# Kernel optimization log

Measured on AMD Instinct MI355X. Metric: run time of the kernel, lower is better.

The kernel has to match this reference:

```python
import jax, jax.numpy as jnp
import numpy as np

B, H, P, L = 16, 128, 64, 8192  # batch, d_input, d_state, seq_len
TWO_PI = 6.283185307179586


def setup_inputs() -> dict:
    key = jax.random.key(0)
    k_u, k_lr, k_li, k_br, k_bi, k_cr, k_ci, k_d = jax.random.split(key, 8)
    u = jax.random.normal(k_u, (B, H, L), dtype=jnp.float32)
    # continuous-time diagonal state matrix: Lambda = -rand + i*2*pi*rand
    lam_re = -jax.random.uniform(k_lr, (P,), dtype=jnp.float32)
    lam_im = TWO_PI * jax.random.uniform(k_li, (P,), dtype=jnp.float32)
    Lam = lam_re + 1j * lam_im                       # (P,) complex64
    Lambda_bar = jnp.exp(Lam)                        # ZOH with Delta=1
    # continuous B, then ZOH: B_bar = (Lambda_bar - 1)/Lambda * B
    Bc = (jax.random.normal(k_br, (P, H), dtype=jnp.float32)
          + 1j * jax.random.normal(k_bi, (P, H), dtype=jnp.float32))
    B_bar = ((Lambda_bar - 1.0) / Lam)[:, None] * Bc  # (P,H) complex64
    C = (jax.random.normal(k_cr, (H, P), dtype=jnp.float32)
         + 1j * jax.random.normal(k_ci, (H, P), dtype=jnp.float32))
    D = jax.random.normal(k_d, (H, H), dtype=jnp.float32)
    return {
        "u": u,
        "Lambda_re": jnp.real(Lambda_bar).astype(jnp.float32),
        "Lambda_im": jnp.imag(Lambda_bar).astype(jnp.float32),
        "B_re": jnp.real(B_bar).astype(jnp.float32),
        "B_im": jnp.imag(B_bar).astype(jnp.float32),
        "C_re": jnp.real(C).astype(jnp.float32),
        "C_im": jnp.imag(C).astype(jnp.float32),
        "D": D,
    }


def _binary_op(elem_i, elem_j):
    # diagonal linear recurrence combine: (A^i, Bu_i) o (A^j, Bu_j)
    a_i, bu_i = elem_i
    a_j, bu_j = elem_j
    return a_j * a_i, a_j * bu_i + bu_j


def reference(u, Lambda_re, Lambda_im, B_re, B_im, C_re, C_im, D):
    Lambda_bar = Lambda_re + 1j * Lambda_im           # (P,)
    B_bar = B_re + 1j * B_im                          # (P,H)
    C = C_re + 1j * C_im                              # (H,P)
    uc = u.astype(B_bar.dtype)                        # (B,H,L) complex
    Bu = jnp.einsum('ph,bhl->bpl', B_bar, uc)         # (B,P,L)
    A = jnp.broadcast_to(Lambda_bar[None, :, None], Bu.shape)
    # parallel associative scan of the diagonal linear recurrence over L
    _, xs = jax.lax.associative_scan(_binary_op, (A, Bu), axis=2)  # (B,P,L)
    C_A_Bu = jnp.einsum('hp,bpl->bhl', C, xs).real    # (B,H,L)
    # einsum('hh,bhl->bhl', D, u) uses only the diagonal of D
    Du = jnp.diagonal(D)[None, :, None] * u           # (B,H,L)
    return jax.nn.gelu(C_A_Bu + Du, approximate=False)
```

## Files before the change

kernel.cpp:

```cpp
#include <hip/hip_runtime.h>
#include <math.h>

#define NB 16
#define NH 128
#define NP 64
#define NL 8192

__global__ __launch_bounds__(256) void k_bu(
    const float* __restrict__ u, const float* __restrict__ Bre,
    const float* __restrict__ Bim, float2* __restrict__ bu) {
  __shared__ float sBre[32][68];
  __shared__ float sBim[32][68];
  __shared__ float sU[32][128];
  const int b  = blockIdx.y;
  const int l0 = blockIdx.x * 128;
  const int t  = threadIdx.x;
  const int tp = t & 15;
  const int tl = t >> 4;
  float accRe[4][8], accIm[4][8];
  #pragma unroll
  for (int i = 0; i < 4; ++i)
    #pragma unroll
    for (int j = 0; j < 8; ++j) { accRe[i][j] = 0.f; accIm[i][j] = 0.f; }

  for (int ht = 0; ht < 4; ++ht) {
    const int h0 = ht * 32;
    #pragma unroll
    for (int idx = t; idx < 2048; idx += 256) {
      int h = idx & 31, p = idx >> 5;
      sBre[h][p] = Bre[p * NH + h0 + h];
      sBim[h][p] = Bim[p * NH + h0 + h];
    }
    #pragma unroll
    for (int idx = t; idx < 32 * 128; idx += 256) {
      int l = idx & 127, h = idx >> 7;
      sU[h][l] = u[((size_t)(b * NH + h0 + h)) * NL + l0 + l];
    }
    __syncthreads();
    #pragma unroll 4
    for (int h = 0; h < 32; ++h) {
      float4 br4 = *(const float4*)&sBre[h][tp * 4];
      float4 bi4 = *(const float4*)&sBim[h][tp * 4];
      float4 ua  = *(const float4*)&sU[h][tl * 8];
      float4 ub  = *(const float4*)&sU[h][tl * 8 + 4];
      float uu[8] = {ua.x, ua.y, ua.z, ua.w, ub.x, ub.y, ub.z, ub.w};
      float brr[4] = {br4.x, br4.y, br4.z, br4.w};
      float bii[4] = {bi4.x, bi4.y, bi4.z, bi4.w};
      #pragma unroll
      for (int i = 0; i < 4; ++i)
        #pragma unroll
        for (int j = 0; j < 8; ++j) {
          accRe[i][j] = fmaf(brr[i], uu[j], accRe[i][j]);
          accIm[i][j] = fmaf(bii[i], uu[j], accIm[i][j]);
        }
    }
    __syncthreads();
  }
  #pragma unroll
  for (int i = 0; i < 4; ++i) {
    size_t base = ((size_t)(b * NP + tp * 4 + i)) * NL + l0 + tl * 8;
    #pragma unroll
    for (int j = 0; j < 8; j += 2) {
      float4 v = make_float4(accRe[i][j], accIm[i][j], accRe[i][j + 1], accIm[i][j + 1]);
      *(float4*)&bu[base + j] = v;
    }
  }
}

__global__ __launch_bounds__(256) void k_scan(
    float2* __restrict__ bu, const float* __restrict__ Lre,
    const float* __restrict__ Lim) {
  extern __shared__ float2 s[];
  const int bp = blockIdx.x;
  const int p  = bp & (NP - 1);
  const int t  = threadIdx.x;
  const size_t base = (size_t)bp * NL;

  float2 v[32];
  #pragma unroll
  for (int j = 0; j < 32; ++j) v[j] = bu[base + t + 256 * j];
  #pragma unroll
  for (int j = 0; j < 32; ++j) { int i = t + 256 * j; s[i + (i >> 5)] = v[j]; }
  __syncthreads();
  #pragma unroll
  for (int j = 0; j < 32; ++j) v[j] = s[t * 33 + j];

  const float lr = Lre[p], li = Lim[p];
  float xr = 0.f, xi = 0.f;
  #pragma unroll
  for (int j = 0; j < 32; ++j) {
    float nr = fmaf(lr, xr, fmaf(-li, xi, v[j].x));
    float ni = fmaf(lr, xi, fmaf( li, xr, v[j].y));
    xr = nr; xi = ni;
    v[j].x = xr; v[j].y = xi;
  }
  __syncthreads();

  float wr = lr, wi = li;
  #pragma unroll
  for (int k = 0; k < 5; ++k) { float nr = wr * wr - wi * wi; wi = 2.f * wr * wi; wr = nr; }
  float2 tot = v[31];
  s[t] = tot;
  __syncthreads();
  for (int d = 1; d < 256; d <<= 1) {
    float2 nb;
    if (t >= d) nb = s[t - d];
    __syncthreads();
    if (t >= d) {
      tot.x += wr * nb.x - wi * nb.y;
      tot.y += wr * nb.y + wi * nb.x;
      s[t] = tot;
    }
    __syncthreads();
    float nr = wr * wr - wi * wi; wi = 2.f * wr * wi; wr = nr;
  }
  float2 ep = (t > 0) ? s[t - 1] : make_float2(0.f, 0.f);
  __syncthreads();

  float cr = ep.x, ci = ep.y;
  #pragma unroll
  for (int j = 0; j < 32; ++j) {
    float nr = lr * cr - li * ci;
    float nc = lr * ci + li * cr;
    cr = nr; ci = nc;
    v[j].x += cr; v[j].y += ci;
  }
  #pragma unroll
  for (int j = 0; j < 32; ++j) s[t * 33 + j] = v[j];
  __syncthreads();
  #pragma unroll
  for (int j = 0; j < 32; ++j) { int i = t + 256 * j; bu[base + i] = s[i + (i >> 5)]; }
}

__global__ __launch_bounds__(256) void k_out(
    const float2* __restrict__ xs, const float* __restrict__ u,
    const float* __restrict__ Cre, const float* __restrict__ Cim,
    const float* __restrict__ D, float* __restrict__ out) {
  __shared__ float sCre[16][132];
  __shared__ float sCim[16][132];
  __shared__ float sXre[16][128];
  __shared__ float sXim[16][128];
  __shared__ float sDd[128];
  const int b  = blockIdx.y;
  const int l0 = blockIdx.x * 128;
  const int t  = threadIdx.x;
  const int lane = t & 63, w = t >> 6;
  const int th = (lane & 7) + 8 * (w & 1);
  const int tl = (lane >> 3) + 8 * (w >> 1);

  if (t < 128) sDd[t] = D[t * NH + t];

  float acc[8][8];
  #pragma unroll
  for (int i = 0; i < 8; ++i)
    #pragma unroll
    for (int j = 0; j < 8; ++j) acc[i][j] = 0.f;

  for (int pt = 0; pt < 4; ++pt) {
    const int p0 = pt * 16;
    __syncthreads();
    #pragma unroll
    for (int idx = t; idx < 2048; idx += 256) {
      int pp = idx & 15, h = idx >> 4;
      sCre[pp][h] = Cre[h * NP + p0 + pp];
      sCim[pp][h] = Cim[h * NP + p0 + pp];
    }
    #pragma unroll
    for (int idx = t; idx < 2048; idx += 256) {
      int l = idx & 127, pp = idx >> 7;
      float2 xv = xs[((size_t)(b * NP + p0 + pp)) * NL + l0 + l];
      sXre[pp][l] = xv.x; sXim[pp][l] = xv.y;
    }
    __syncthreads();
    #pragma unroll 4
    for (int pp = 0; pp < 16; ++pp) {
      float4 ca = *(const float4*)&sCre[pp][th * 8];
      float4 cb = *(const float4*)&sCre[pp][th * 8 + 4];
      float4 ia = *(const float4*)&sCim[pp][th * 8];
      float4 ib = *(const float4*)&sCim[pp][th * 8 + 4];
      float4 xa = *(const float4*)&sXre[pp][tl * 8];
      float4 xb = *(const float4*)&sXre[pp][tl * 8 + 4];
      float4 ya = *(const float4*)&sXim[pp][tl * 8];
      float4 yb = *(const float4*)&sXim[pp][tl * 8 + 4];
      float cr[8] = {ca.x, ca.y, ca.z, ca.w, cb.x, cb.y, cb.z, cb.w};
      float ci[8] = {ia.x, ia.y, ia.z, ia.w, ib.x, ib.y, ib.z, ib.w};
      float xr[8] = {xa.x, xa.y, xa.z, xa.w, xb.x, xb.y, xb.z, xb.w};
      float xi[8] = {ya.x, ya.y, ya.z, ya.w, yb.x, yb.y, yb.z, yb.w};
      #pragma unroll
      for (int i = 0; i < 8; ++i)
        #pragma unroll
        for (int j = 0; j < 8; ++j) {
          acc[i][j] = fmaf(cr[i], xr[j], acc[i][j]);
          acc[i][j] = fmaf(-ci[i], xi[j], acc[i][j]);
        }
    }
  }

  #pragma unroll
  for (int i = 0; i < 8; ++i) {
    const int h = th * 8 + i;
    const float dd = sDd[h];
    size_t rb = ((size_t)(b * NH + h)) * NL + l0 + tl * 8;
    float4 u0 = *(const float4*)&u[rb];
    float4 u1 = *(const float4*)&u[rb + 4];
    float uu[8] = {u0.x, u0.y, u0.z, u0.w, u1.x, u1.y, u1.z, u1.w};
    float r[8];
    #pragma unroll
    for (int j = 0; j < 8; ++j) {
      float vv = acc[i][j] + dd * uu[j];
      r[j] = 0.5f * vv * (1.0f + erff(vv * 0.70710678118654752f));
    }
    *(float4*)&out[rb]     = make_float4(r[0], r[1], r[2], r[3]);
    *(float4*)&out[rb + 4] = make_float4(r[4], r[5], r[6], r[7]);
  }
}

extern "C" void kernel_launch(void* const* d_in, const int* in_sizes, int n_in,
                              void* d_out, int out_size, void* d_ws, size_t ws_size,
                              hipStream_t stream) {
  (void)in_sizes; (void)n_in; (void)out_size; (void)ws_size;
  const float* u   = (const float*)d_in[0];
  const float* Lre = (const float*)d_in[1];
  const float* Lim = (const float*)d_in[2];
  const float* Bre = (const float*)d_in[3];
  const float* Bim = (const float*)d_in[4];
  const float* Cre = (const float*)d_in[5];
  const float* Cim = (const float*)d_in[6];
  const float* Dm  = (const float*)d_in[7];
  float* out = (float*)d_out;
  float2* bu = (float2*)d_ws;

  dim3 g1(NL / 128, NB);
  k_bu<<<g1, 256, 0, stream>>>(u, Bre, Bim, bu);
  k_scan<<<NB * NP, 256, 8448 * sizeof(float2), stream>>>(bu, Lre, Lim);
  dim3 g3(NL / 128, NB);
  k_out<<<g3, 256, 0, stream>>>(bu, u, Cre, Cim, Dm, out);
}
```

Measured before the change: 302.5 us.

## Fuse chunked local scan into Bu GEMM and apply carries in output kernel

Result: faster. 264.0 us (-12.7%).

```diff
diff --git a/kernel.cpp b/kernel.cpp
--- a/kernel.cpp
+++ b/kernel.cpp
@@ -5,15 +5,19 @@
 #define NH 128
 #define NP 64
 #define NL 8192
-
-__global__ __launch_bounds__(256) void k_bu(
+#define NCHUNK 64
+
+__global__ __launch_bounds__(256) void k_bu_scan(
     const float* __restrict__ u, const float* __restrict__ Bre,
-    const float* __restrict__ Bim, float2* __restrict__ bu) {
-  __shared__ float sBre[32][68];
+    const float* __restrict__ Bim, const float* __restrict__ Lre,
+    const float* __restrict__ Lim, float2* __restrict__ xloc,
+    float2* __restrict__ Echunk) {
+  __shared__ __align__(16) float sBre[32][68];
   __shared__ float sBim[32][68];
   __shared__ float sU[32][128];
   const int b  = blockIdx.y;
-  const int l0 = blockIdx.x * 128;
+  const int c  = blockIdx.x;
+  const int l0 = c * 128;
   const int t  = threadIdx.x;
   const int tp = t & 15;
   const int tl = t >> 4;
@@ -56,97 +60,138 @@
     }
     __syncthreads();
   }
+
+  float lr[4], li[4];
+  #pragma unroll
+  for (int i = 0; i < 4; ++i) { lr[i] = Lre[tp * 4 + i]; li[i] = Lim[tp * 4 + i]; }
+  #pragma unroll
+  for (int i = 0; i < 4; ++i) {
+    float xr = 0.f, xi = 0.f;
+    #pragma unroll
+    for (int j = 0; j < 8; ++j) {
+      float nr = fmaf(lr[i], xr, fmaf(-li[i], xi, accRe[i][j]));
+      float ni = fmaf(lr[i], xi, fmaf( li[i], xr, accIm[i][j]));
+      xr = nr; xi = ni; accRe[i][j] = xr; accIm[i][j] = xi;
+    }
+  }
+
+  float2* E = reinterpret_cast<float2*>(&sBre[0][0]);
+  #define EL(p, q) E[(p) * 17 + (q)]
+  #pragma unroll
+  for (int i = 0; i < 4; ++i)
+    EL(tp * 4 + i, tl) = make_float2(accRe[i][7], accIm[i][7]);
+
+  float wr[4], wi[4];
+  #pragma unroll
+  for (int i = 0; i < 4; ++i) {
+    float ar = lr[i], ai = li[i];
+    #pragma unroll
+    for (int k = 0; k < 3; ++k) { float nr = ar * ar - ai * ai; ai = 2.f * ar * ai; ar = nr; }
+    wr[i] = ar; wi[i] = ai;
+  }
+  __syncthreads();
+  #pragma unroll
+  for (int d = 1; d < 16; d <<= 1) {
+    float2 rv[4];
+    #pragma unroll
+    for (int i = 0; i < 4; ++i)
+      rv[i] = (tl >= d) ? EL(tp * 4 + i, tl - d) : make_float2(0.f, 0.f);
+    __syncthreads();
+    if (tl >= d) {
+      #pragma unroll
+      for (int i = 0; i < 4; ++i) {
+        float2 cur = EL(tp * 4 + i, tl);
+        cur.x += wr[i] * rv[i].x - wi[i] * rv[i].y;
+        cur.y += wr[i] * rv[i].y + wi[i] * rv[i].x;
+        EL(tp * 4 + i, tl) = cur;
+      }
+    }
+    __syncthreads();
+    #pragma unroll
+    for (int i = 0; i < 4; ++i) {
+      float nr = wr[i] * wr[i] - wi[i] * wi[i];
+      wi[i] = 2.f * wr[i] * wi[i]; wr[i] = nr;
+    }
+  }
+
+  float2 cin[4];
+  #pragma unroll
+  for (int i = 0; i < 4; ++i)
+    cin[i] = (tl > 0) ? EL(tp * 4 + i, tl - 1) : make_float2(0.f, 0.f);
+  if (t < 64) {
+    float2 tot = EL(t, 15);
+    Echunk[((size_t)(b * NCHUNK + c)) * NP + t] = tot;
+  }
+
+  #pragma unroll
+  for (int i = 0; i < 4; ++i) {
+    float cr = cin[i].x, ci = cin[i].y;
+    #pragma unroll
+    for (int j = 0; j < 8; ++j) {
+      float nr = lr[i] * cr - li[i] * ci;
+      float nc = lr[i] * ci + li[i] * cr;
+      cr = nr; ci = nc;
+      accRe[i][j] += cr; accIm[i][j] += ci;
+    }
+  }
+
   #pragma unroll
   for (int i = 0; i < 4; ++i) {
     size_t base = ((size_t)(b * NP + tp * 4 + i)) * NL + l0 + tl * 8;
     #pragma unroll
     for (int j = 0; j < 8; j += 2) {
       float4 v = make_float4(accRe[i][j], accIm[i][j], accRe[i][j + 1], accIm[i][j + 1]);
-      *(float4*)&bu[base + j] = v;
-    }
-  }
+      *(float4*)&xloc[base + j] = v;
+    }
+  }
+  #undef EL
 }
 
-__global__ __launch_bounds__(256) void k_scan(
-    float2* __restrict__ bu, const float* __restrict__ Lre,
-    const float* __restrict__ Lim) {
-  extern __shared__ float2 s[];
-  const int bp = blockIdx.x;
-  const int p  = bp & (NP - 1);
-  const int t  = threadIdx.x;
-  const size_t base = (size_t)bp * NL;
-
-  float2 v[32];
-  #pragma unroll
-  for (int j = 0; j < 32; ++j) v[j] = bu[base + t + 256 * j];
-  #pragma unroll
-  for (int j = 0; j < 32; ++j) { int i = t + 256 * j; s[i + (i >> 5)] = v[j]; }
-  __syncthreads();
-  #pragma unroll
-  for (int j = 0; j < 32; ++j) v[j] = s[t * 33 + j];
-
+__global__ void k_carry(const float2* __restrict__ Echunk,
+                        const float* __restrict__ Lre, const float* __restrict__ Lim,
+                        float2* __restrict__ carryg, float2* __restrict__ powtab) {
+  const int b = blockIdx.x, p = threadIdx.x;
   const float lr = Lre[p], li = Lim[p];
+  float wr = lr, wi = li;
+  #pragma unroll
+  for (int k = 0; k < 7; ++k) { float nr = wr * wr - wi * wi; wi = 2.f * wr * wi; wr = nr; }
   float xr = 0.f, xi = 0.f;
-  #pragma unroll
-  for (int j = 0; j < 32; ++j) {
-    float nr = fmaf(lr, xr, fmaf(-li, xi, v[j].x));
-    float ni = fmaf(lr, xi, fmaf( li, xr, v[j].y));
+  for (int c = 0; c < NCHUNK; ++c) {
+    carryg[((size_t)(b * NCHUNK + c)) * NP + p] = make_float2(xr, xi);
+    float2 e = Echunk[((size_t)(b * NCHUNK + c)) * NP + p];
+    float nr = e.x + wr * xr - wi * xi;
+    float ni = e.y + wr * xi + wi * xr;
     xr = nr; xi = ni;
-    v[j].x = xr; v[j].y = xi;
-  }
-  __syncthreads();
-
-  float wr = lr, wi = li;
-  #pragma unroll
-  for (int k = 0; k < 5; ++k) { float nr = wr * wr - wi * wi; wi = 2.f * wr * wi; wr = nr; }
-  float2 tot = v[31];
-  s[t] = tot;
-  __syncthreads();
-  for (int d = 1; d < 256; d <<= 1) {
-    float2 nb;
-    if (t >= d) nb = s[t - d];
-    __syncthreads();
-    if (t >= d) {
-      tot.x += wr * nb.x - wi * nb.y;
-      tot.y += wr * nb.y + wi * nb.x;
-      s[t] = tot;
-    }
-    __syncthreads();
-    float nr = wr * wr - wi * wi; wi = 2.f * wr * wi; wr = nr;
-  }
-  float2 ep = (t > 0) ? s[t - 1] : make_float2(0.f, 0.f);
-  __syncthreads();
-
-  float cr = ep.x, ci = ep.y;
-  #pragma unroll
-  for (int j = 0; j < 32; ++j) {
-    float nr = lr * cr - li * ci;
-    float nc = lr * ci + li * cr;
-    cr = nr; ci = nc;
-    v[j].x += cr; v[j].y += ci;
-  }
-  #pragma unroll
-  for (int j = 0; j < 32; ++j) s[t * 33 + j] = v[j];
-  __syncthreads();
-  #pragma unroll
-  for (int j = 0; j < 32; ++j) { int i = t + 256 * j; bu[base + i] = s[i + (i >> 5)]; }
+  }
+  if (b == 0) {
+    float pr = 1.f, pi = 0.f;
+    for (int j = 0; j < 128; ++j) {
+      float nr = pr * lr - pi * li;
+      pi = pr * li + pi * lr; pr = nr;
+      powtab[p * 128 + j] = make_float2(pr, pi);
+    }
+  }
 }
 
 __global__ __launch_bounds__(256) void k_out(
     const float2* __restrict__ xs, const float* __restrict__ u,
     const float* __restrict__ Cre, const float* __restrict__ Cim,
-    const float* __restrict__ D, float* __restrict__ out) {
+    const float* __restrict__ D, const float2* __restrict__ carryg,
+    const float2* __restrict__ powtab, float* __restrict__ out) {
   __shared__ float sCre[16][132];
   __shared__ float sCim[16][132];
   __shared__ float sXre[16][128];
   __shared__ float sXim[16][128];
   __shared__ float sDd[128];
   const int b  = blockIdx.y;
-  const int l0 = blockIdx.x * 128;
+  const int c  = blockIdx.x;
+  const int l0 = c * 128;
   const int t  = threadIdx.x;
   const int lane = t & 63, w = t >> 6;
   const int th = (lane & 7) + 8 * (w & 1);
   const int tl = (lane >> 3) + 8 * (w >> 1);
+  const int lfix = t & 127;
+  const int ppb  = t >> 7;
 
   if (t < 128) sDd[t] = D[t * NH + t];
 
@@ -156,6 +201,16 @@
     #pragma unroll
     for (int j = 0; j < 8; ++j) acc[i][j] = 0.f;
 
+  float2 gx[8], gp[8], gc[8];
+  #pragma unroll
+  for (int k = 0; k < 8; ++k) {
+    int pp = ppb + 2 * k;
+    gx[k] = xs[((size_t)(b * NP + pp)) * NL + l0 + lfix];
+    gp[k] = powtab[pp * 128 + lfix];
+    gc[k] = carryg[((size_t)(b * NCHUNK + c)) * NP + pp];
+  }
+
+  #pragma unroll
   for (int pt = 0; pt < 4; ++pt) {
     const int p0 = pt * 16;
     __syncthreads();
@@ -166,12 +221,23 @@
       sCim[pp][h] = Cim[h * NP + p0 + pp];
     }
     #pragma unroll
-    for (int idx = t; idx < 2048; idx += 256) {
-      int l = idx & 127, pp = idx >> 7;
-      float2 xv = xs[((size_t)(b * NP + p0 + pp)) * NL + l0 + l];
-      sXre[pp][l] = xv.x; sXim[pp][l] = xv.y;
-    }
-    __syncthreads();
+    for (int k = 0; k < 8; ++k) {
+      int pp = ppb + 2 * k;
+      float xr = gx[k].x + gp[k].x * gc[k].x - gp[k].y * gc[k].y;
+      float xi = gx[k].y + gp[k].x * gc[k].y + gp[k].y * gc[k].x;
+      sXre[pp][lfix] = xr; sXim[pp][lfix] = xi;
+    }
+    __syncthreads();
+    if (pt < 3) {
+      const int p1 = (pt + 1) * 16;
+      #pragma unroll
+      for (int k = 0; k < 8; ++k) {
+        int pp = ppb + 2 * k;
+        gx[k] = xs[((size_t)(b * NP + p1 + pp)) * NL + l0 + lfix];
+        gp[k] = powtab[(p1 + pp) * 128 + lfix];
+        gc[k] = carryg[((size_t)(b * NCHUNK + c)) * NP + p1 + pp];
+      }
+    }
     #pragma unroll 4
     for (int pp = 0; pp < 16; ++pp) {
       float4 ca = *(const float4*)&sCre[pp][th * 8];
@@ -228,11 +294,15 @@
   const float* Cim = (const float*)d_in[6];
   const float* Dm  = (const float*)d_in[7];
   float* out = (float*)d_out;
-  float2* bu = (float2*)d_ws;
-
-  dim3 g1(NL / 128, NB);
-  k_bu<<<g1, 256, 0, stream>>>(u, Bre, Bim, bu);
-  k_scan<<<NB * NP, 256, 8448 * sizeof(float2), stream>>>(bu, Lre, Lim);
-  dim3 g3(NL / 128, NB);
-  k_out<<<g3, 256, 0, stream>>>(bu, u, Cre, Cim, Dm, out);
+
+  char* wsb = (char*)d_ws;
+  float2* xloc   = (float2*)wsb;
+  float2* Echunk = (float2*)(wsb + 67108864);
+  float2* carryg = (float2*)(wsb + 67108864 + 524288);
+  float2* powtab = (float2*)(wsb + 67108864 + 1048576);
+
+  dim3 g(NL / 128, NB);
+  k_bu_scan<<<g, 256, 0, stream>>>(u, Bre, Bim, Lre, Lim, xloc, Echunk);
+  k_carry<<<NB, NP, 0, stream>>>(Echunk, Lre, Lim, carryg, powtab);
+  k_out<<<g, 256, 0, stream>>>(xloc, u, Cre, Cim, Dm, carryg, powtab, out);
 }
```
